# Kernel tuning notes

Hardware: AMD Instinct MI355X
Metric: run time of the kernel (lower is better)

Reference implementation:

```python
import jax, jax.numpy as jnp
import numpy as np

B, H, N, C, E, D, L_OUT, LAYERS = 16, 64, 512, 3, 128, 32, 12, 2


def setup_inputs() -> dict:
    key = jax.random.key(0)
    ks = jax.random.split(key, 16)
    nrm = lambda k, s, sc=1.0: jax.random.normal(k, s, jnp.float32) * sc
    adj = jax.random.uniform(ks[0], (N, N), jnp.float32)
    adj = adj / adj.sum(axis=-1, keepdims=True)  # row-normalized prior adjacency
    return {
        "x_input": nrm(ks[1], (B, H, N, C)),
        "adj": adj,
        "Wf": nrm(ks[2], (3, E, 3 * C), 0.1),
        "Uf": nrm(ks[3], (3, E, E), 0.05),
        "bf": jnp.zeros((3, E), jnp.float32),
        "E1f": nrm(ks[4], (N, D)),
        "E2f": nrm(ks[5], (N, D)),
        "Wb": nrm(ks[6], (3, E, 3 * C), 0.1),
        "Ub": nrm(ks[7], (3, E, E), 0.05),
        "bb": jnp.zeros((3, E), jnp.float32),
        "E1b": nrm(ks[8], (N, D)),
        "E2b": nrm(ks[9], (N, D)),
        "dec_w": nrm(ks[10], (L_OUT, LAYERS, 2 * E), 0.05),  # Conv2d(layer_num->out_len, k=(1,2E)) squeezed
        "dec_b": jnp.zeros((L_OUT,), jnp.float32),
        "out_w": nrm(ks[11], (L_OUT, L_OUT), 0.1),  # 1x1 Conv2d squeezed
        "out_b": jnp.zeros((L_OUT,), jnp.float32),
    }


def _cell_step(c, xt, adj, A_dyn, W, U, b):
    # Graph-coupled GRU cell (IBNCell): xt [B,C,N], c [B,E,N].
    msg = jnp.concatenate(
        [xt,
         jnp.einsum('bcn,nm->bcm', xt, adj),      # prior-graph message passing
         jnp.einsum('bcn,nm->bcm', xt, A_dyn)],   # learned dynamic-graph message passing
        axis=1)  # [B, 3C, N]
    gx = jnp.einsum('goc,bcn->gbon', W, msg)  # 3 stacked gate projections
    r = jax.nn.sigmoid(gx[0] + jnp.einsum('oe,ben->bon', U[0], c) + b[0][:, None])
    u = jax.nn.sigmoid(gx[1] + jnp.einsum('oe,ben->bon', U[1], c) + b[1][:, None])
    g = jnp.tanh(gx[2] + jnp.einsum('oe,ben->bon', U[2], r * c) + b[2][:, None])
    return u * c + (1.0 - u) * g


def _forward(x_input, adj, Wf, Uf, bf, E1f, E2f, Wb, Ub, bb, E1b, E2b, dec_w, dec_b, out_w, out_b):
    # torch: x_input.transpose(-3,-1).transpose(-2,-1) -> [B,C,H,N]; scan layout [H,B,C,N]
    xs = jnp.transpose(x_input, (1, 0, 3, 2))
    A_f = jax.nn.softmax(jax.nn.relu(E1f @ E2f.T), axis=-1)  # dynamic adjacency, fwd cell
    A_b = jax.nn.softmax(jax.nn.relu(E1b @ E2b.T), axis=-1)  # dynamic adjacency, back cell
    c0 = jnp.zeros((xs.shape[1], Wf.shape[1], xs.shape[3]), xs.dtype)  # [B,E,N]

    def step_f(c, xt):
        cn = _cell_step(c, xt, adj, A_f, Wf, Uf, bf)
        return cn, None

    # Output only depends on the last timestep of the bidirectional concat:
    # forward branch -> final state after H steps; backward branch (after flip)
    # at t=H-1 -> its FIRST step (input x[H-1]). Dead per-step outputs elided.
    h_fwd, _ = jax.lax.scan(step_f, c0, xs)
    h_back0 = _cell_step(c0, xs[-1], adj, A_b, Wb, Ub, bb)
    last_ht = jnp.concatenate([h_fwd, h_back0], axis=1)  # [B, 2E, N]

    lt = jnp.transpose(last_ht, (0, 2, 1))  # [B, N, 2E]
    # layer loop z>0 is a no-op on current_layer_output -> final_result repeats last_ht
    final = jnp.broadcast_to(lt[:, None], (lt.shape[0], LAYERS, lt.shape[1], lt.shape[2]))
    h = jnp.einsum('blne,ole->bon', final, dec_w) + dec_b[:, None]  # decoder conv (1,2E)
    return jnp.einsum('oi,bin->bon', out_w, h) + out_b[:, None]  # 1x1 output conv -> [B,L_OUT,N]


def reference(x_input, adj, Wf, Uf, bf, E1f, E2f, Wb, Ub, bb, E1b, E2b, dec_w, dec_b, out_w, out_b):
    return _forward(x_input, adj, Wf, Uf, bf, E1f, E2f, Wb, Ub, bb, E1b, E2b, dec_w, dec_b, out_w, out_b)
```

## Files before the change

kernel.cpp:

```cpp
#include <hip/hip_runtime.h>


typedef _Float16 half8_t __attribute__((ext_vector_type(8)));
typedef __fp16 fp16x2_t __attribute__((ext_vector_type(2)));
typedef float float4_t __attribute__((ext_vector_type(4)));

#define PIN(x) asm volatile("" : "+v"(x))

__device__ __forceinline__ float exp2_(float x) { return __builtin_amdgcn_exp2f(x); }
__device__ __forceinline__ float rcp_(float x) { return __builtin_amdgcn_rcpf(x); }

__global__ __launch_bounds__(256) void prep_kernel(
    const float* __restrict__ E1f, const float* __restrict__ E2f,
    const float* __restrict__ E1b, const float* __restrict__ E2b,
    const float* __restrict__ adj, const float* __restrict__ Wf,
    const float* __restrict__ Uf, const float* __restrict__ bf,
    const float* __restrict__ Wb, const float* __restrict__ bb,
    _Float16* __restrict__ adjT, _Float16* __restrict__ AfT,
    _Float16* __restrict__ AbT, _Float16* __restrict__ ufrag,
    _Float16* __restrict__ wbfrag) {
  int bid = blockIdx.x;
  int tid = threadIdx.x;
  if (bid >= 1272) {
    int r2 = bid - 1272;
    int gi = 1 + (r2 & 1);
    int og = r2 >> 1;
    float scl = (gi == 2) ? 2.8853902f : -1.4426950f;
    for (int e = tid; e < 512; e += 256) {
      int lane = e >> 3, j = e & 7;
      int o = og * 16 + (lane & 15);
      int q = (lane >> 4) * 8 + j;
      float v = (q < 9) ? Wb[gi * 1152 + o * 9 + q]
                        : (q == 9 ? bb[gi * 128 + o] : 0.f);
      wbfrag[r2 * 512 + e] = (_Float16)(v * scl);
    }
    return;
  }
  if (bid >= 1152) {
    int r = bid - 1152;
    int kb = r % 5;
    int gi = (r / 5) % 3;
    int og = r / 15;
    float scl = (gi == 2) ? 2.8853902f : -1.4426950f;
    for (int e = tid; e < 512; e += 256) {
      int lane = e >> 3, j = e & 7;
      int o = og * 16 + (lane & 15);
      int q4 = lane >> 4;
      float v;
      if (kb < 4) {
        v = Uf[gi * 16384 + o * 128 + kb * 32 + q4 * 8 + j];
      } else {
        int q = q4 * 8 + j;
        v = (q < 9) ? Wf[gi * 1152 + o * 9 + q]
                    : (q == 9 ? bf[gi * 128 + o] : 0.f);
      }
      ufrag[r * 512 + e] = (_Float16)(v * scl);
    }
    return;
  }
  if (bid >= 1024) {
    int base = (bid - 1024) * 4;
    for (int r = 0; r < 4; ++r) {
      int row = base + r;
      float v0 = adj[row * 512 + tid];
      float v1 = adj[row * 512 + tid + 256];
      adjT[(size_t)tid * 512 + row] = (_Float16)v0;
      adjT[(size_t)(tid + 256) * 512 + row] = (_Float16)v1;
    }
    return;
  }
  int which = bid >> 9;
  int row = bid & 511;
  const float* E1 = which ? E1b : E1f;
  const float* E2 = which ? E2b : E2f;
  _Float16* A = which ? AbT : AfT;
  __shared__ float e1s[32];
  __shared__ float red[256];
  if (tid < 32) e1s[tid] = E1[row * 32 + tid];
  __syncthreads();
  float s[2];
#pragma unroll
  for (int h = 0; h < 2; ++h) {
    int m = tid + h * 256;
    const float4* e2 = (const float4*)(E2 + m * 32);
    float acc = 0.f;
#pragma unroll
    for (int d4 = 0; d4 < 8; ++d4) {
      float4 v = e2[d4];
      acc = fmaf(v.x, e1s[d4 * 4 + 0], acc);
      acc = fmaf(v.y, e1s[d4 * 4 + 1], acc);
      acc = fmaf(v.z, e1s[d4 * 4 + 2], acc);
      acc = fmaf(v.w, e1s[d4 * 4 + 3], acc);
    }
    s[h] = fmaxf(acc, 0.f);
  }
  red[tid] = fmaxf(s[0], s[1]);
  __syncthreads();
  for (int off = 128; off > 0; off >>= 1) {
    if (tid < off) red[tid] = fmaxf(red[tid], red[tid + off]);
    __syncthreads();
  }
  float mx = red[0];
  __syncthreads();
  float e0 = __expf(s[0] - mx), e1v = __expf(s[1] - mx);
  red[tid] = e0 + e1v;
  __syncthreads();
  for (int off = 128; off > 0; off >>= 1) {
    if (tid < off) red[tid] += red[tid + off];
    __syncthreads();
  }
  float inv = rcp_(red[0]);
  A[(size_t)tid * 512 + row] = (_Float16)(e0 * inv);
  A[(size_t)(tid + 256) * 512 + row] = (_Float16)(e1v * inv);
}

__global__ __launch_bounds__(256, 2) void msg_kernel(
    const float* __restrict__ x, const _Float16* __restrict__ adjT,
    const _Float16* __restrict__ AfT, const _Float16* __restrict__ AbT,
    _Float16* __restrict__ msgF, _Float16* __restrict__ msgbF) {
  __shared__ __align__(16) _Float16 Alds[48 * 512];
  __shared__ __align__(16) _Float16 Sst[16 * 4 * 32 * 8];
  int tid = threadIdx.x;
  int t = blockIdx.x >> 3;
  int n0g = (blockIdx.x & 7) * 64;
  int g4 = (blockIdx.x & 7) * 4;
  int lane = tid & 63, og = tid >> 6;
  int l15 = lane & 15, q4 = lane >> 4, q0 = q4 * 8;
  bool is63 = (t == 63);

  {
    int b = tid >> 4, li = tid & 15;
    const float4* xb = (const float4*)(x + (size_t)(b * 64 + t) * 1536);
#pragma unroll
    for (int k = 0; k < 24; ++k) {
      float4 v = xb[k * 16 + li];
      int j0 = (k * 16 + li) * 4;
#pragma unroll
      for (int e = 0; e < 4; ++e) {
        int j = j0 + e;
        int n = (j * 21846) >> 16;
        int c = j - n * 3;
        int m = b * 3 + c;
        float val = (e == 0) ? v.x : (e == 1) ? v.y : (e == 2) ? v.z : v.w;
        Alds[m * 512 + ((((n >> 3) ^ (m & 7)) << 3) | (n & 7))] = (_Float16)val;
      }
    }
  }
  __syncthreads();

  const float4_t zero4 = {0.f, 0.f, 0.f, 0.f};
  float4_t acc[3][2], accb[3];
#pragma unroll
  for (int mt = 0; mt < 3; ++mt) { acc[mt][0] = zero4; acc[mt][1] = zero4; accb[mt] = zero4; }

  int n = n0g + og * 16 + l15;
  for (int kb = 0; kb < 16; ++kb) {
    half8_t afr[3];
#pragma unroll
    for (int mt = 0; mt < 3; ++mt) {
      int m = mt * 16 + l15;
      afr[mt] = *(const half8_t*)&Alds[m * 512 + ((((kb * 4 + q4) ^ (m & 7)) << 3))];
    }
    half8_t b0 = *(const half8_t*)&adjT[(size_t)n * 512 + kb * 32 + q0];
    half8_t b1 = *(const half8_t*)&AfT[(size_t)n * 512 + kb * 32 + q0];
#pragma unroll
    for (int mt = 0; mt < 3; ++mt) {
      acc[mt][0] = __builtin_amdgcn_mfma_f32_16x16x32_f16(afr[mt], b0, acc[mt][0], 0, 0, 0);
      acc[mt][1] = __builtin_amdgcn_mfma_f32_16x16x32_f16(afr[mt], b1, acc[mt][1], 0, 0, 0);
    }
    if (is63) {
      half8_t b2 = *(const half8_t*)&AbT[(size_t)n * 512 + kb * 32 + q0];
#pragma unroll
      for (int mt = 0; mt < 3; ++mt)
        accb[mt] = __builtin_amdgcn_mfma_f32_16x16x32_f16(afr[mt], b2, accb[mt], 0, 0, 0);
    }
  }

  for (int u = tid; u < 1024; u += 256) {
    int tb = u >> 6, nt = (u >> 4) & 3, cl = u & 15;
    int nn = n0g + nt * 16 + cl;
    _Float16* r0 = &Sst[(((tb * 4 + nt) * 32) + cl) * 8];
    _Float16* r1 = r0 + 16 * 8;
#pragma unroll
    for (int c = 0; c < 3; ++c) {
      int m = tb * 3 + c;
      r0[c] = Alds[m * 512 + ((((nn >> 3) ^ (m & 7)) << 3) | (nn & 7))];
    }
    r1[1] = (_Float16)1.f;
#pragma unroll
    for (int z = 2; z < 8; ++z) r1[z] = (_Float16)0.f;
  }
#pragma unroll
  for (int mt = 0; mt < 3; ++mt)
#pragma unroll
    for (int r = 0; r < 4; ++r) {
      int m = mt * 16 + q4 * 4 + r;
      int tb = (m * 21846) >> 16;
      int ch = m - tb * 3;
      _Float16* base = &Sst[((tb * 4 + og) * 32) * 8];
      base[(l15)*8 + 3 + ch] = (_Float16)acc[mt][0][r];
      if (ch < 2) base[(l15)*8 + 6 + ch] = (_Float16)acc[mt][1][r];
      else        base[(16 + l15) * 8 + 0] = (_Float16)acc[mt][1][r];
    }
  __syncthreads();
  for (int i = tid; i < 2048; i += 256) {
    int sl = i >> 5, lane32 = i & 31;
    int tb = sl >> 2, nt = sl & 3;
    ((uint4*)msgF)[((size_t)(tb * 32 + g4 + nt) * 64 + t) * 32 + lane32] =
        ((const uint4*)Sst)[i];
  }
  if (is63) {
    __syncthreads();
#pragma unroll
    for (int mt = 0; mt < 3; ++mt)
#pragma unroll
      for (int r = 0; r < 4; ++r) {
        int m = mt * 16 + q4 * 4 + r;
        int tb = (m * 21846) >> 16;
        int ch = m - tb * 3;
        _Float16* base = &Sst[((tb * 4 + og) * 32) * 8];
        if (ch < 2) base[(l15)*8 + 6 + ch] = (_Float16)accb[mt][r];
        else        base[(16 + l15) * 8 + 0] = (_Float16)accb[mt][r];
      }
    __syncthreads();
    for (int i = tid; i < 2048; i += 256) {
      int sl = i >> 5, lane32 = i & 31;
      int tb = sl >> 2, nt = sl & 3;
      ((uint4*)msgbF)[(size_t)(tb * 32 + g4 + nt) * 32 + lane32] =
          ((const uint4*)Sst)[i];
    }
  }
}

__global__ __launch_bounds__(512, 4) void rec_kernel(
    const _Float16* __restrict__ msgF, const _Float16* __restrict__ msgbF,
    const _Float16* __restrict__ ufrag, const _Float16* __restrict__ wbfrag,
    const float* __restrict__ dec_w, const float* __restrict__ dec_b,
    const float* __restrict__ out_w, const float* __restrict__ out_b,
    float* __restrict__ out) {
  __shared__ __align__(16) _Float16 Cbuf[2048];
  __shared__ __align__(16) _Float16 Gbuf[2048];
  __shared__ float hf_lds[128 * 16];
  __shared__ float hb_lds[128 * 16];
  __shared__ float hdec_lds[12 * 16];
  int tid = threadIdx.x, bid = blockIdx.x;
  int b = bid >> 5;
  int nt = bid & 31;
  int n0 = nt * 16;
  int lane = tid & 63, og = tid >> 6;
  int l15 = lane & 15, q4 = lane >> 4;

  half8_t afrag[3][5];
#pragma unroll
  for (int gi = 0; gi < 3; ++gi)
#pragma unroll
    for (int kb = 0; kb < 5; ++kb) {
      afrag[gi][kb] = *(const half8_t*)
          &ufrag[(size_t)(((og * 3 + gi) * 5 + kb) * 512) + lane * 8];
      PIN(afrag[gi][kb]);
    }

  if (tid < 256) {
    uint4 z; z.x = z.y = z.z = z.w = 0;
    ((uint4*)Cbuf)[tid] = z;
  }
  float cr[4] = {0.f, 0.f, 0.f, 0.f};

  const float4_t zero4 = {0.f, 0.f, 0.f, 0.f};
  union H4U { fp16x2_t h2[2]; unsigned long long u; };
  const _Float16* mp = msgF + (size_t)(b * 32 + nt) * 64 * 256 + (lane & 31) * 8;
  half8_t bm = *(const half8_t*)mp;

  int kb_w = og >> 1;
  int lane_w = ((og & 1) * 2 + (q4 >> 1)) * 16 + l15;
  int j0 = (q4 & 1) * 4;
  __syncthreads();

  for (int t = 0; t < 64; ++t) {
    mp += 256;
    half8_t bm_n = *(const half8_t*)mp;

    half8_t cf[4];
#pragma unroll
    for (int kb = 0; kb < 4; ++kb)
      cf[kb] = *(const half8_t*)&Cbuf[(kb * 64 + lane) * 8];

    float4_t accr = zero4, accu = zero4;
#pragma unroll
    for (int kb = 0; kb < 4; ++kb) {
      accr = __builtin_amdgcn_mfma_f32_16x16x32_f16(afrag[0][kb], cf[kb], accr, 0, 0, 0);
      accu = __builtin_amdgcn_mfma_f32_16x16x32_f16(afrag[1][kb], cf[kb], accu, 0, 0, 0);
    }
    accr = __builtin_amdgcn_mfma_f32_16x16x32_f16(afrag[0][4], bm, accr, 0, 0, 0);
    accu = __builtin_amdgcn_mfma_f32_16x16x32_f16(afrag[1][4], bm, accu, 0, 0, 0);
    float4_t accg = __builtin_amdgcn_mfma_f32_16x16x32_f16(afrag[2][4], bm, zero4, 0, 0, 0);

    {
      float rc0 = rcp_(1.f + exp2_(accr[0])) * cr[0];
      float rc1 = rcp_(1.f + exp2_(accr[1])) * cr[1];
      float rc2 = rcp_(1.f + exp2_(accr[2])) * cr[2];
      float rc3 = rcp_(1.f + exp2_(accr[3])) * cr[3];
      H4U v;
      v.h2[0] = __builtin_amdgcn_cvt_pkrtz(rc0, rc1);
      v.h2[1] = __builtin_amdgcn_cvt_pkrtz(rc2, rc3);
      *(unsigned long long*)&Gbuf[(kb_w * 64 + lane_w) * 8 + j0] = v.u;
    }
    __syncthreads();

    half8_t gf[4];
#pragma unroll
    for (int kb = 0; kb < 4; ++kb)
      gf[kb] = *(const half8_t*)&Gbuf[(kb * 64 + lane) * 8];
#pragma unroll
    for (int kb = 0; kb < 4; ++kb)
      accg = __builtin_amdgcn_mfma_f32_16x16x32_f16(afrag[2][kb], gf[kb], accg, 0, 0, 0);

    {
      H4U v;
      float cn[4];
#pragma unroll
      for (int r = 0; r < 4; ++r) {
        float uu = rcp_(1.f + exp2_(accu[r]));
        float gg = fmaf(-2.f, rcp_(exp2_(accg[r]) + 1.f), 1.f);
        cn[r] = fmaf(uu, cr[r] - gg, gg);
        cr[r] = cn[r];
      }
      v.h2[0] = __builtin_amdgcn_cvt_pkrtz(cn[0], cn[1]);
      v.h2[1] = __builtin_amdgcn_cvt_pkrtz(cn[2], cn[3]);
      *(unsigned long long*)&Cbuf[(kb_w * 64 + lane_w) * 8 + j0] = v.u;
    }
    __syncthreads();
    bm = bm_n;
  }

  {
    half8_t bbk = *(const half8_t*)
        (msgbF + (size_t)(b * 32 + nt) * 256 + (lane & 31) * 8);
    half8_t au_f = *(const half8_t*)&wbfrag[(size_t)((og * 2 + 0) * 512) + lane * 8];
    half8_t ag_f = *(const half8_t*)&wbfrag[(size_t)((og * 2 + 1) * 512) + lane * 8];
    float4_t au = __builtin_amdgcn_mfma_f32_16x16x32_f16(au_f, bbk, zero4, 0, 0, 0);
    float4_t ag = __builtin_amdgcn_mfma_f32_16x16x32_f16(ag_f, bbk, zero4, 0, 0, 0);
#pragma unroll
    for (int r = 0; r < 4; ++r) {
      int row = og * 16 + q4 * 4 + r;
      float uu = rcp_(1.f + exp2_(au[r]));
      float gg = fmaf(-2.f, rcp_(exp2_(ag[r]) + 1.f), 1.f);
      hb_lds[row * 16 + l15] = (1.f - uu) * gg;
      hf_lds[row * 16 + l15] = cr[r];
    }
  }
  __syncthreads();

  if (tid < 192) {
    int i = tid >> 4, cc = tid & 15;
    const float* dwa = dec_w + (size_t)i * 512;
    const float* dwb = dwa + 256;
    float hd = dec_b[i];
    for (int e = 0; e < 128; ++e) {
      hd = fmaf(dwa[e] + dwb[e], hf_lds[e * 16 + cc], hd);
      hd = fmaf(dwa[128 + e] + dwb[128 + e], hb_lds[e * 16 + cc], hd);
    }
    hdec_lds[i * 16 + cc] = hd;
  }
  __syncthreads();
  if (tid < 192) {
    int o = tid >> 4, cc = tid & 15;
    float v = out_b[o];
#pragma unroll
    for (int i = 0; i < 12; ++i) v = fmaf(out_w[o * 12 + i], hdec_lds[i * 16 + cc], v);
    out[((size_t)(b * 12 + o)) * 512 + n0 + cc] = v;
  }
}

extern "C" void kernel_launch(void* const* d_in, const int* in_sizes, int n_in,
                              void* d_out, int out_size, void* d_ws, size_t ws_size,
                              hipStream_t stream) {
  (void)in_sizes; (void)n_in; (void)out_size; (void)ws_size;
  const float* x     = (const float*)d_in[0];
  const float* adj   = (const float*)d_in[1];
  const float* Wf    = (const float*)d_in[2];
  const float* Uf    = (const float*)d_in[3];
  const float* bf    = (const float*)d_in[4];
  const float* E1f   = (const float*)d_in[5];
  const float* E2f   = (const float*)d_in[6];
  const float* Wb    = (const float*)d_in[7];
  const float* bb    = (const float*)d_in[9];
  const float* E1b   = (const float*)d_in[10];
  const float* E2b   = (const float*)d_in[11];
  const float* dec_w = (const float*)d_in[12];
  const float* dec_b = (const float*)d_in[13];
  const float* out_w = (const float*)d_in[14];
  const float* out_b = (const float*)d_in[15];

  _Float16* h      = (_Float16*)d_ws;
  _Float16* adjT   = h;
  _Float16* AfT    = h + 262144;
  _Float16* AbT    = h + 524288;
  _Float16* ufrag  = h + 786432;
  _Float16* wbfrag = h + 847872;
  _Float16* msgF   = h + 856064;
  _Float16* msgbF  = h + 9244672;

  prep_kernel<<<1288, 256, 0, stream>>>(E1f, E2f, E1b, E2b, adj, Wf, Uf, bf,
                                        Wb, bb, adjT, AfT, AbT, ufrag, wbfrag);
  msg_kernel<<<512, 256, 0, stream>>>(x, adjT, AfT, AbT, msgF, msgbF);
  rec_kernel<<<512, 512, 0, stream>>>(msgF, msgbF, ufrag, wbfrag,
                                      dec_w, dec_b, out_w, out_b, (float*)d_out);
}
```

Measured before the change: 203.0 us.

## Store messages as dense 16-half rows and read zero padding from shared pad

```diff
diff --git a/kernel.cpp b/kernel.cpp
--- a/kernel.cpp
+++ b/kernel.cpp
@@ -18,9 +18,13 @@
     const float* __restrict__ Wb, const float* __restrict__ bb,
     _Float16* __restrict__ adjT, _Float16* __restrict__ AfT,
     _Float16* __restrict__ AbT, _Float16* __restrict__ ufrag,
-    _Float16* __restrict__ wbfrag) {
+    _Float16* __restrict__ wbfrag, _Float16* __restrict__ zpad) {
   int bid = blockIdx.x;
   int tid = threadIdx.x;
+  if (bid >= 1288) {
+    if (tid < 64) zpad[tid] = (_Float16)0.f;
+    return;
+  }
   if (bid >= 1272) {
     int r2 = bid - 1272;
     int gi = 1 + (r2 & 1);
@@ -117,13 +121,12 @@
 __global__ __launch_bounds__(256, 2) void msg_kernel(
     const float* __restrict__ x, const _Float16* __restrict__ adjT,
     const _Float16* __restrict__ AfT, const _Float16* __restrict__ AbT,
-    _Float16* __restrict__ msgF, _Float16* __restrict__ msgbF) {
+    _Float16* __restrict__ msg16, _Float16* __restrict__ msgb16) {
   __shared__ __align__(16) _Float16 Alds[48 * 512];
-  __shared__ __align__(16) _Float16 Sst[16 * 4 * 32 * 8];
+  __shared__ __align__(16) _Float16 Sst[1024 * 16];
   int tid = threadIdx.x;
   int t = blockIdx.x >> 3;
   int n0g = (blockIdx.x & 7) * 64;
-  int g4 = (blockIdx.x & 7) * 4;
   int lane = tid & 63, og = tid >> 6;
   int l15 = lane & 15, q4 = lane >> 4, q0 = q4 * 8;
   bool is63 = (t == 63);
@@ -176,19 +179,18 @@
     }
   }
 
-  for (int u = tid; u < 1024; u += 256) {
-    int tb = u >> 6, nt = (u >> 4) & 3, cl = u & 15;
-    int nn = n0g + nt * 16 + cl;
-    _Float16* r0 = &Sst[(((tb * 4 + nt) * 32) + cl) * 8];
-    _Float16* r1 = r0 + 16 * 8;
+  for (int i = tid; i < 1024; i += 256) {
+    int tb = i >> 6, nl = i & 63;
+    int nn = n0g + nl;
+    _Float16* row = &Sst[i * 16];
 #pragma unroll
     for (int c = 0; c < 3; ++c) {
       int m = tb * 3 + c;
-      r0[c] = Alds[m * 512 + ((((nn >> 3) ^ (m & 7)) << 3) | (nn & 7))];
-    }
-    r1[1] = (_Float16)1.f;
-#pragma unroll
-    for (int z = 2; z < 8; ++z) r1[z] = (_Float16)0.f;
+      row[c] = Alds[m * 512 + ((((nn >> 3) ^ (m & 7)) << 3) | (nn & 7))];
+    }
+    row[9] = (_Float16)1.f;
+#pragma unroll
+    for (int z = 10; z < 16; ++z) row[z] = (_Float16)0.f;
   }
 #pragma unroll
   for (int mt = 0; mt < 3; ++mt)
@@ -196,17 +198,16 @@
     for (int r = 0; r < 4; ++r) {
       int m = mt * 16 + q4 * 4 + r;
       int tb = (m * 21846) >> 16;
-      int ch = m - tb * 3;
-      _Float16* base = &Sst[((tb * 4 + og) * 32) * 8];
-      base[(l15)*8 + 3 + ch] = (_Float16)acc[mt][0][r];
-      if (ch < 2) base[(l15)*8 + 6 + ch] = (_Float16)acc[mt][1][r];
-      else        base[(16 + l15) * 8 + 0] = (_Float16)acc[mt][1][r];
+      int c = m - tb * 3;
+      _Float16* row = &Sst[(tb * 64 + og * 16 + l15) * 16];
+      row[3 + c] = (_Float16)acc[mt][0][r];
+      row[6 + c] = (_Float16)acc[mt][1][r];
     }
   __syncthreads();
   for (int i = tid; i < 2048; i += 256) {
-    int sl = i >> 5, lane32 = i & 31;
-    int tb = sl >> 2, nt = sl & 3;
-    ((uint4*)msgF)[((size_t)(tb * 32 + g4 + nt) * 64 + t) * 32 + lane32] =
+    int rrow = i >> 1, h = i & 1;
+    int tb = rrow >> 6, nl = rrow & 63;
+    ((uint4*)msg16)[(((size_t)(t * 16 + tb) * 512) + n0g + nl) * 2 + h] =
         ((const uint4*)Sst)[i];
   }
   if (is63) {
@@ -217,27 +218,25 @@
       for (int r = 0; r < 4; ++r) {
         int m = mt * 16 + q4 * 4 + r;
         int tb = (m * 21846) >> 16;
-        int ch = m - tb * 3;
-        _Float16* base = &Sst[((tb * 4 + og) * 32) * 8];
-        if (ch < 2) base[(l15)*8 + 6 + ch] = (_Float16)accb[mt][r];
-        else        base[(16 + l15) * 8 + 0] = (_Float16)accb[mt][r];
+        int c = m - tb * 3;
+        Sst[(tb * 64 + og * 16 + l15) * 16 + 6 + c] = (_Float16)accb[mt][r];
       }
     __syncthreads();
     for (int i = tid; i < 2048; i += 256) {
-      int sl = i >> 5, lane32 = i & 31;
-      int tb = sl >> 2, nt = sl & 3;
-      ((uint4*)msgbF)[(size_t)(tb * 32 + g4 + nt) * 32 + lane32] =
+      int rrow = i >> 1, h = i & 1;
+      int tb = rrow >> 6, nl = rrow & 63;
+      ((uint4*)msgb16)[(((size_t)tb * 512) + n0g + nl) * 2 + h] =
           ((const uint4*)Sst)[i];
     }
   }
 }
 
 __global__ __launch_bounds__(512, 4) void rec_kernel(
-    const _Float16* __restrict__ msgF, const _Float16* __restrict__ msgbF,
-    const _Float16* __restrict__ ufrag, const _Float16* __restrict__ wbfrag,
-    const float* __restrict__ dec_w, const float* __restrict__ dec_b,
-    const float* __restrict__ out_w, const float* __restrict__ out_b,
-    float* __restrict__ out) {
+    const _Float16* __restrict__ msg16, const _Float16* __restrict__ msgb16,
+    const _Float16* __restrict__ zpad, const _Float16* __restrict__ ufrag,
+    const _Float16* __restrict__ wbfrag, const float* __restrict__ dec_w,
+    const float* __restrict__ dec_b, const float* __restrict__ out_w,
+    const float* __restrict__ out_b, float* __restrict__ out) {
   __shared__ __align__(16) _Float16 Cbuf[2048];
   __shared__ __align__(16) _Float16 Gbuf[2048];
   __shared__ float hf_lds[128 * 16];
@@ -268,8 +267,11 @@
 
   const float4_t zero4 = {0.f, 0.f, 0.f, 0.f};
   union H4U { fp16x2_t h2[2]; unsigned long long u; };
-  const _Float16* mp = msgF + (size_t)(b * 32 + nt) * 64 * 256 + (lane & 31) * 8;
-  half8_t bm = *(const half8_t*)mp;
+  const char* base = (const char*)msg16 +
+                     ((size_t)(b * 512 + n0 + l15)) * 32 + (q4 & 1) * 16;
+  const char* mrow = (q4 < 2) ? base : (const char*)zpad;
+  size_t tstr = (q4 < 2) ? (size_t)16 * 512 * 32 : 0;
+  half8_t bm = *(const half8_t*)mrow;
 
   int kb_w = og >> 1;
   int lane_w = ((og & 1) * 2 + (q4 >> 1)) * 16 + l15;
@@ -277,8 +279,8 @@
   __syncthreads();
 
   for (int t = 0; t < 64; ++t) {
-    mp += 256;
-    half8_t bm_n = *(const half8_t*)mp;
+    int tn = (t < 63) ? t + 1 : 63;
+    half8_t bm_n = *(const half8_t*)(mrow + (size_t)tn * tstr);
 
     half8_t cf[4];
 #pragma unroll
@@ -293,17 +295,20 @@
     }
     accr = __builtin_amdgcn_mfma_f32_16x16x32_f16(afrag[0][4], bm, accr, 0, 0, 0);
     accu = __builtin_amdgcn_mfma_f32_16x16x32_f16(afrag[1][4], bm, accu, 0, 0, 0);
-    float4_t accg = __builtin_amdgcn_mfma_f32_16x16x32_f16(afrag[2][4], bm, zero4, 0, 0, 0);
-
+    float4_t accg_p = __builtin_amdgcn_mfma_f32_16x16x32_f16(afrag[2][4], bm, zero4, 0, 0, 0);
+
+    float uu[4];
     {
-      float rc0 = rcp_(1.f + exp2_(accr[0])) * cr[0];
-      float rc1 = rcp_(1.f + exp2_(accr[1])) * cr[1];
-      float rc2 = rcp_(1.f + exp2_(accr[2])) * cr[2];
-      float rc3 = rcp_(1.f + exp2_(accr[3])) * cr[3];
       H4U v;
-      v.h2[0] = __builtin_amdgcn_cvt_pkrtz(rc0, rc1);
-      v.h2[1] = __builtin_amdgcn_cvt_pkrtz(rc2, rc3);
+#pragma unroll
+      for (int r = 0; r < 2; ++r) {
+        float a = rcp_(1.f + exp2_(accr[2 * r])) * cr[2 * r];
+        float bq = rcp_(1.f + exp2_(accr[2 * r + 1])) * cr[2 * r + 1];
+        v.h2[r] = __builtin_amdgcn_cvt_pkrtz(a, bq);
+      }
       *(unsigned long long*)&Gbuf[(kb_w * 64 + lane_w) * 8 + j0] = v.u;
+#pragma unroll
+      for (int r = 0; r < 4; ++r) uu[r] = rcp_(1.f + exp2_(accu[r]));
     }
     __syncthreads();
 
@@ -311,6 +316,7 @@
 #pragma unroll
     for (int kb = 0; kb < 4; ++kb)
       gf[kb] = *(const half8_t*)&Gbuf[(kb * 64 + lane) * 8];
+    float4_t accg = accg_p;
 #pragma unroll
     for (int kb = 0; kb < 4; ++kb)
       accg = __builtin_amdgcn_mfma_f32_16x16x32_f16(afrag[2][kb], gf[kb], accg, 0, 0, 0);
@@ -320,9 +326,8 @@
       float cn[4];
 #pragma unroll
       for (int r = 0; r < 4; ++r) {
-        float uu = rcp_(1.f + exp2_(accu[r]));
         float gg = fmaf(-2.f, rcp_(exp2_(accg[r]) + 1.f), 1.f);
-        cn[r] = fmaf(uu, cr[r] - gg, gg);
+        cn[r] = fmaf(uu[r], cr[r] - gg, gg);
         cr[r] = cn[r];
       }
       v.h2[0] = __builtin_amdgcn_cvt_pkrtz(cn[0], cn[1]);
@@ -334,8 +339,10 @@
   }
 
   {
-    half8_t bbk = *(const half8_t*)
-        (msgbF + (size_t)(b * 32 + nt) * 256 + (lane & 31) * 8);
+    const char* bb_base = (const char*)msgb16 +
+                          ((size_t)(b * 512 + n0 + l15)) * 32 + (q4 & 1) * 16;
+    const char* bp = (q4 < 2) ? bb_base : (const char*)zpad;
+    half8_t bbk = *(const half8_t*)bp;
     half8_t au_f = *(const half8_t*)&wbfrag[(size_t)((og * 2 + 0) * 512) + lane * 8];
     half8_t ag_f = *(const half8_t*)&wbfrag[(size_t)((og * 2 + 1) * 512) + lane * 8];
     float4_t au = __builtin_amdgcn_mfma_f32_16x16x32_f16(au_f, bbk, zero4, 0, 0, 0);
@@ -343,9 +350,9 @@
 #pragma unroll
     for (int r = 0; r < 4; ++r) {
       int row = og * 16 + q4 * 4 + r;
-      float uu = rcp_(1.f + exp2_(au[r]));
+      float uu2 = rcp_(1.f + exp2_(au[r]));
       float gg = fmaf(-2.f, rcp_(exp2_(ag[r]) + 1.f), 1.f);
-      hb_lds[row * 16 + l15] = (1.f - uu) * gg;
+      hb_lds[row * 16 + l15] = (1.f - uu2) * gg;
       hf_lds[row * 16 + l15] = cr[r];
     }
   }
@@ -398,12 +405,13 @@
   _Float16* AbT    = h + 524288;
   _Float16* ufrag  = h + 786432;
   _Float16* wbfrag = h + 847872;
-  _Float16* msgF   = h + 856064;
-  _Float16* msgbF  = h + 9244672;
-
-  prep_kernel<<<1288, 256, 0, stream>>>(E1f, E2f, E1b, E2b, adj, Wf, Uf, bf,
-                                        Wb, bb, adjT, AfT, AbT, ufrag, wbfrag);
-  msg_kernel<<<512, 256, 0, stream>>>(x, adjT, AfT, AbT, msgF, msgbF);
-  rec_kernel<<<512, 512, 0, stream>>>(msgF, msgbF, ufrag, wbfrag,
+  _Float16* zpad   = h + 856064;
+  _Float16* msg16  = h + 856128;
+  _Float16* msgb16 = h + 9244736;
+
+  prep_kernel<<<1289, 256, 0, stream>>>(E1f, E2f, E1b, E2b, adj, Wf, Uf, bf,
+                                        Wb, bb, adjT, AfT, AbT, ufrag, wbfrag, zpad);
+  msg_kernel<<<512, 256, 0, stream>>>(x, adjT, AfT, AbT, msg16, msgb16);
+  rec_kernel<<<512, 512, 0, stream>>>(msg16, msgb16, zpad, ufrag, wbfrag,
                                       dec_w, dec_b, out_w, out_b, (float*)d_out);
 }
```

Measured after the change: 200.5 us. About the same (-1.3%).
